# Optimization experiments

Hardware: AMD Instinct MI355X
Metric: run time of the kernel (lower is better)

## Reference

```python
import jax, jax.numpy as jnp
import numpy as np

EPS = 1e-5
BETA = 0.2

def _conv(x, w, b, stride, pad):
    y = jax.lax.conv_general_dilated(x, w, (stride, stride), ((pad, pad), (pad, pad)),
                                     dimension_numbers=('NCHW', 'OIHW', 'NCHW'))
    return y + b[None, :, None, None]

def _convT(x, w, b, stride, pad_eq):
    # PyTorch ConvTranspose2d(k=4, s=2, p=1) == dilated conv with lhs_dilation=s,
    # padding k-1-p=2, with the (already generated) equivalent OIHW kernel.
    y = jax.lax.conv_general_dilated(x, w, (1, 1), ((pad_eq, pad_eq), (pad_eq, pad_eq)),
                                     lhs_dilation=(stride, stride),
                                     dimension_numbers=('NCHW', 'OIHW', 'NCHW'))
    return y + b[None, :, None, None]

def _bn(x, g, b):
    # training-mode BatchNorm2d: batch statistics over (N,H,W), biased variance
    m = jnp.mean(x, axis=(0, 2, 3), keepdims=True)
    v = jnp.mean((x - m) ** 2, axis=(0, 2, 3), keepdims=True)
    return g[None, :, None, None] * (x - m) * jax.lax.rsqrt(v + EPS) + b[None, :, None, None]

def setup_inputs() -> dict:
    key = jax.random.key(0)
    ks = jax.random.split(key, 12)
    d = {}
    d['x'] = jax.random.normal(ks[0], (64, 1, 256, 256), jnp.float32)
    d['enc_w1'] = jax.random.normal(ks[1], (16, 1, 4, 4), jnp.float32) * 0.1
    d['enc_b1'] = jnp.zeros((16,), jnp.float32)
    d['bn1_g'] = jnp.ones((16,), jnp.float32)
    d['bn1_b'] = jnp.zeros((16,), jnp.float32)
    d['enc_w2'] = jax.random.normal(ks[2], (4, 16, 4, 4), jnp.float32) * 0.05
    d['enc_b2'] = jnp.zeros((4,), jnp.float32)
    d['bn2_g'] = jnp.ones((4,), jnp.float32)
    d['bn2_b'] = jnp.zeros((4,), jnp.float32)
    d['pre_w'] = jax.random.normal(ks[3], (2, 4, 1, 1), jnp.float32) * 0.3
    d['pre_b'] = jnp.zeros((2,), jnp.float32)
    d['codebook'] = jax.random.normal(ks[4], (3, 2), jnp.float32)
    d['post_w'] = jax.random.normal(ks[5], (4, 2, 1, 1), jnp.float32) * 0.3
    d['post_b'] = jnp.zeros((4,), jnp.float32)
    d['dec_w1'] = jax.random.normal(ks[6], (16, 4, 4, 4), jnp.float32) * 0.1
    d['dec_b1'] = jnp.zeros((16,), jnp.float32)
    d['bn3_g'] = jnp.ones((16,), jnp.float32)
    d['bn3_b'] = jnp.zeros((16,), jnp.float32)
    d['dec_w2'] = jax.random.normal(ks[7], (1, 16, 4, 4), jnp.float32) * 0.1
    d['dec_b2'] = jnp.zeros((1,), jnp.float32)
    return d

def reference(x, enc_w1, enc_b1, bn1_g, bn1_b, enc_w2, enc_b2, bn2_g, bn2_b,
              pre_w, pre_b, codebook, post_w, post_b,
              dec_w1, dec_b1, bn3_g, bn3_b, dec_w2, dec_b2):
    # encoder
    h = jax.nn.relu(_bn(_conv(x, enc_w1, enc_b1, 2, 1), bn1_g, bn1_b))
    h = jax.nn.relu(_bn(_conv(h, enc_w2, enc_b2, 2, 1), bn2_g, bn2_b))
    z = _conv(h, pre_w, pre_b, 1, 0)                      # [B,2,H/4,W/4]
    B, C, H, W = z.shape
    zf = z.reshape(B, C, H * W).transpose(0, 2, 1)        # [B, N, C]
    # squared distances to codebook [K,C]; argmin same as cdist argmin
    d2 = (jnp.sum(zf ** 2, -1, keepdims=True)
          - 2.0 * jnp.einsum('bnc,kc->bnk', zf, codebook)
          + jnp.sum(codebook ** 2, -1))                   # [B,N,K]
    idx = jnp.argmin(d2, axis=-1)                         # [B,N]
    q = codebook[idx]                                     # [B,N,C]
    commitment_loss = jnp.mean((jax.lax.stop_gradient(q) - zf) ** 2)
    codebook_loss = jnp.mean((q - jax.lax.stop_gradient(zf)) ** 2)
    quantize_losses = codebook_loss + BETA * commitment_loss
    q_st = zf + jax.lax.stop_gradient(q - zf)             # straight-through
    q4d = q_st.transpose(0, 2, 1).reshape(B, C, H, W)
    # decoder
    h = _conv(q4d, post_w, post_b, 1, 0)
    h = jax.nn.relu(_bn(_convT(h, dec_w1, dec_b1, 2, 2), bn3_g, bn3_b))
    out = _convT(h, dec_w2, dec_b2, 2, 2)                 # [B,1,256,256]
    return out, quantize_losses
```

## Files before the change

kernel.cpp:

```cpp
#include <hip/hip_runtime.h>


__global__ __launch_bounds__(256) void k_conv1(
    const float* __restrict__ x, const float* __restrict__ w1,
    const float* __restrict__ b1, float* __restrict__ y1,
    float* __restrict__ part)
{
  __shared__ float s_w[256];
  __shared__ float s_b[16];
  const int tid = threadIdx.x;
  { int c = tid >> 4, k = tid & 15; s_w[k * 16 + c] = w1[c * 16 + k]; }
  if (tid < 16) s_b[tid] = b1[tid];
  __syncthreads();

  const int lane = tid & 63;
  const int cb = lane & 3;
  const int psl = lane >> 2;
  const int gwave = (blockIdx.x << 2) | (tid >> 6);
  const int base = gwave << 8;
  const int n = base >> 14;
  const float* xb = x + n * 65536;
  const float4* s_w4 = (const float4*)s_w;
  const float4 bv = ((const float4*)s_b)[cb];

  float lsum[4] = {0.f, 0.f, 0.f, 0.f}, lsq[4] = {0.f, 0.f, 0.f, 0.f};

#pragma unroll 1
  for (int i = 0; i < 16; ++i) {
    const int pos = base + (i << 4) + psl;
    const int r = pos & 16383;
    const int oh = r >> 7, ow = r & 127;
    const int ihb = oh * 2 - 1, iwb = ow * 2 - 1;

    float a0 = bv.x, a1 = bv.y, a2 = bv.z, a3 = bv.w;
#pragma unroll
    for (int kh = 0; kh < 4; ++kh) {
      int ih = ihb + kh; bool okh = (unsigned)ih < 256u;
#pragma unroll
      for (int kw = 0; kw < 4; ++kw) {
        int iw = iwb + kw;
        bool ok = okh && ((unsigned)iw < 256u);
        float v = ok ? xb[ih * 256 + iw] : 0.f;
        float4 wv = s_w4[(kh * 4 + kw) * 4 + cb];
        a0 = fmaf(v, wv.x, a0); a1 = fmaf(v, wv.y, a1);
        a2 = fmaf(v, wv.z, a2); a3 = fmaf(v, wv.w, a3);
      }
    }
    *(float4*)(y1 + (size_t)pos * 16 + cb * 4) = make_float4(a0, a1, a2, a3);
    lsum[0] += a0; lsum[1] += a1; lsum[2] += a2; lsum[3] += a3;
    lsq[0] = fmaf(a0, a0, lsq[0]); lsq[1] = fmaf(a1, a1, lsq[1]);
    lsq[2] = fmaf(a2, a2, lsq[2]); lsq[3] = fmaf(a3, a3, lsq[3]);
  }

#pragma unroll
  for (int j = 0; j < 4; ++j) {
    float sv = lsum[j], qv = lsq[j];
#pragma unroll
    for (int d = 4; d < 64; d <<= 1) { sv += __shfl_down(sv, d); qv += __shfl_down(qv, d); }
    if (lane < 4) {
      part[(lane * 4 + j) * 4096 + gwave]      = sv;
      part[(16 + lane * 4 + j) * 4096 + gwave] = qv;
    }
  }
}

template <int NCH, int NW>
__global__ __launch_bounds__(256) void k_bnredN(
    const float* __restrict__ part, const float* __restrict__ g,
    const float* __restrict__ bt, float* __restrict__ sc,
    float* __restrict__ sh, double invN)
{
  __shared__ double sd[256], sqd[256];
  const int c = blockIdx.x, tid = threadIdx.x;
  const float4* ps = (const float4*)(part + (size_t)c * NW);
  const float4* pq = (const float4*)(part + (size_t)(NCH + c) * NW);
  double S = 0.0, Q = 0.0;
#pragma unroll
  for (int i = 0; i < NW / 1024; ++i) {
    float4 v = ps[i * 256 + tid];
    S += (double)v.x + (double)v.y + (double)v.z + (double)v.w;
    float4 q = pq[i * 256 + tid];
    Q += (double)q.x + (double)q.y + (double)q.z + (double)q.w;
  }
  sd[tid] = S; sqd[tid] = Q;
  __syncthreads();
  for (int off = 128; off > 0; off >>= 1) {
    if (tid < off) { sd[tid] += sd[tid + off]; sqd[tid] += sqd[tid + off]; }
    __syncthreads();
  }
  if (tid == 0) {
    double mean = sd[0] * invN;
    double var  = sqd[0] * invN - mean * mean;
    float scale = (float)((double)g[c] / sqrt(var + 1e-5));
    sc[c] = scale;
    sh[c] = bt[c] - (float)mean * scale;
  }
}

__global__ __launch_bounds__(256) void k_conv2(
    const float* __restrict__ y1, const float* __restrict__ w2,
    const float* __restrict__ b2, const float* __restrict__ bnp,
    float* __restrict__ y2, float* __restrict__ part)
{
  __shared__ float s_w[1024];
  __shared__ float s_sc[16], s_sh[16];
  __shared__ float s_b[4];
  const int tid = threadIdx.x;
  for (int i = tid; i < 1024; i += 256) {
    int co = i & 3, ci = (i >> 2) & 15, k = i >> 6;
    int kh = k >> 2, kw = k & 3;
    s_w[i] = w2[((co * 16 + ci) * 4 + kh) * 4 + kw];
  }
  if (tid < 16) { s_sc[tid] = bnp[tid]; s_sh[tid] = bnp[16 + tid]; }
  if (tid < 4)  s_b[tid] = b2[tid];
  __syncthreads();

  const int bid = ((blockIdx.x & 7) << 9) | (blockIdx.x >> 3);
  const int lane = tid & 63;
  const int cb = lane & 3;
  const int psl = lane >> 2;
  const int gwave = (bid << 2) | (tid >> 6);
  const int pos = (gwave << 4) + psl;
  const int n = pos >> 12, r = pos & 4095;
  const int oh = r >> 6, ow = r & 63;
  const int ihb = oh * 2 - 1, iwb = ow * 2 - 1;
  const float* yb = y1 + (size_t)n * 262144;
  const float4* s_w4 = (const float4*)s_w;
  const float4 scv = ((const float4*)s_sc)[cb];
  const float4 shv = ((const float4*)s_sh)[cb];

  float acc0 = 0.f, acc1 = 0.f, acc2 = 0.f, acc3 = 0.f;

#pragma unroll
  for (int kh = 0; kh < 4; ++kh) {
    int ih = ihb + kh; bool okh = (unsigned)ih < 128u;
#pragma unroll
    for (int kw = 0; kw < 4; ++kw) {
      int iw = iwb + kw;
      bool ok = okh && ((unsigned)iw < 128u);
      if (ok) {
        float4 v = *(const float4*)(yb + (ih * 128 + iw) * 16 + (cb << 2));
        float a0 = fmaxf(fmaf(v.x, scv.x, shv.x), 0.f);
        float a1 = fmaxf(fmaf(v.y, scv.y, shv.y), 0.f);
        float a2 = fmaxf(fmaf(v.z, scv.z, shv.z), 0.f);
        float a3 = fmaxf(fmaf(v.w, scv.w, shv.w), 0.f);
        int kb = (((kh << 2) | kw) << 4) + (cb << 2);
        float4 w0 = s_w4[kb + 0];
        float4 w1 = s_w4[kb + 1];
        float4 w2v = s_w4[kb + 2];
        float4 w3 = s_w4[kb + 3];
        acc0 = fmaf(a0, w0.x, fmaf(a1, w1.x, fmaf(a2, w2v.x, fmaf(a3, w3.x, acc0))));
        acc1 = fmaf(a0, w0.y, fmaf(a1, w1.y, fmaf(a2, w2v.y, fmaf(a3, w3.y, acc1))));
        acc2 = fmaf(a0, w0.z, fmaf(a1, w1.z, fmaf(a2, w2v.z, fmaf(a3, w3.z, acc2))));
        acc3 = fmaf(a0, w0.w, fmaf(a1, w1.w, fmaf(a2, w2v.w, fmaf(a3, w3.w, acc3))));
      }
    }
  }
  acc0 += __shfl_xor(acc0, 1); acc0 += __shfl_xor(acc0, 2);
  acc1 += __shfl_xor(acc1, 1); acc1 += __shfl_xor(acc1, 2);
  acc2 += __shfl_xor(acc2, 1); acc2 += __shfl_xor(acc2, 2);
  acc3 += __shfl_xor(acc3, 1); acc3 += __shfl_xor(acc3, 2);
  acc0 += s_b[0]; acc1 += s_b[1]; acc2 += s_b[2]; acc3 += s_b[3];

  if (cb == 0)
    *(float4*)(y2 + (size_t)pos * 4) = make_float4(acc0, acc1, acc2, acc3);

  float ls[4] = {acc0, acc1, acc2, acc3};
#pragma unroll
  for (int c = 0; c < 4; ++c) {
    float sv = ls[c], qv = ls[c] * ls[c];
#pragma unroll
    for (int d = 4; d < 64; d <<= 1) { sv += __shfl_down(sv, d); qv += __shfl_down(qv, d); }
    if (lane == 0) {
      part[c * 16384 + gwave]       = sv;
      part[(4 + c) * 16384 + gwave] = qv;
    }
  }
}

__global__ __launch_bounds__(256) void k_vq(
    const float* __restrict__ y2, const float* __restrict__ bnp2,
    const float* __restrict__ pw, const float* __restrict__ pb,
    const float* __restrict__ cb, const float* __restrict__ postw,
    const float* __restrict__ postb, float* __restrict__ h3,
    float* __restrict__ lpart)
{
  const int tid = threadIdx.x;
  const int pos = blockIdx.x * 256 + tid;
  float4 v = *(const float4*)(y2 + (size_t)pos * 4);
  float aa0 = fmaxf(fmaf(v.x, bnp2[0], bnp2[4]), 0.f);
  float aa1 = fmaxf(fmaf(v.y, bnp2[1], bnp2[5]), 0.f);
  float aa2 = fmaxf(fmaf(v.z, bnp2[2], bnp2[6]), 0.f);
  float aa3 = fmaxf(fmaf(v.w, bnp2[3], bnp2[7]), 0.f);
  float z0 = pb[0] + aa0*pw[0] + aa1*pw[1] + aa2*pw[2] + aa3*pw[3];
  float z1 = pb[1] + aa0*pw[4] + aa1*pw[5] + aa2*pw[6] + aa3*pw[7];

  float best = 3.4e38f, q0 = 0.f, q1 = 0.f;
#pragma unroll
  for (int k = 0; k < 3; ++k) {
    float c0 = cb[2 * k], c1 = cb[2 * k + 1];
    float dx = z0 - c0, dy = z1 - c1;
    float d = dx * dx + dy * dy;
    if (d < best) { best = d; q0 = c0; q1 = c1; }
  }
  float dl = (q0 - z0) * (q0 - z0) + (q1 - z1) * (q1 - z1);

  float4 hv;
  hv.x = fmaf(q0, postw[0], fmaf(q1, postw[1], postb[0]));
  hv.y = fmaf(q0, postw[2], fmaf(q1, postw[3], postb[1]));
  hv.z = fmaf(q0, postw[4], fmaf(q1, postw[5], postb[2]));
  hv.w = fmaf(q0, postw[6], fmaf(q1, postw[7], postb[3]));
  *(float4*)(h3 + (size_t)pos * 4) = hv;

  float s = dl;
#pragma unroll
  for (int d = 32; d > 0; d >>= 1) s += __shfl_down(s, d);
  __shared__ float ws4[4];
  if ((tid & 63) == 0) ws4[tid >> 6] = s;
  __syncthreads();
  if (tid == 0) lpart[blockIdx.x] = (ws4[0] + ws4[1]) + (ws4[2] + ws4[3]);
}

__global__ __launch_bounds__(256) void k_lossfin(
    const float* __restrict__ lpart, float* __restrict__ outp)
{
  const int tid = threadIdx.x;
  float s = lpart[tid] + lpart[tid + 256] + lpart[tid + 512] + lpart[tid + 768];
#pragma unroll
  for (int d = 32; d > 0; d >>= 1) s += __shfl_down(s, d);
  __shared__ float ws4[4];
  if ((tid & 63) == 0) ws4[tid >> 6] = s;
  __syncthreads();
  if (tid == 0) {
    double tot = (double)ws4[0] + (double)ws4[1] + (double)ws4[2] + (double)ws4[3];
    outp[0] = (float)(1.2 * tot / 524288.0);
  }
}

__global__ __launch_bounds__(256) void k_convt1(
    const float* __restrict__ h3, const float* __restrict__ w,
    const float* __restrict__ bias, float* __restrict__ h4,
    float* __restrict__ part)
{
  __shared__ float s_w[1024];
  __shared__ float s_b[16];
  const int tid = threadIdx.x;
  for (int i = tid; i < 1024; i += 256) {
    int co = i & 15, ci = (i >> 4) & 3, k = i >> 6;
    int kh = k >> 2, kw = k & 3;
    s_w[i] = w[((co * 4 + ci) * 4 + kh) * 4 + kw];
  }
  if (tid < 16) s_b[tid] = bias[tid];
  __syncthreads();

  const int lane = tid & 63;
  const int cb = lane & 3;
  const int psl = lane >> 2;
  const int gwave = (blockIdx.x << 2) | (tid >> 6);
  const int base = gwave << 8;
  const int n = base >> 14;
  const float* hb = h3 + (size_t)n * 16384;
  const float4* s_w4 = (const float4*)s_w;
  const float4 bv = ((const float4*)s_b)[cb];

  float lsum[4] = {0.f, 0.f, 0.f, 0.f}, lsq[4] = {0.f, 0.f, 0.f, 0.f};

#pragma unroll 1
  for (int i = 0; i < 16; ++i) {
    const int pos = base + (i << 4) + psl;
    const int r = pos & 16383;
    const int oh = r >> 7, ow = r & 127;
    const int ohp = oh & 1, owp = ow & 1;

    float a0 = bv.x, a1 = bv.y, a2 = bv.z, a3 = bv.w;
#pragma unroll
    for (int th = 0; th < 2; ++th) {
      int kh = th * 2 + ohp;
      int ih = (oh + kh - 2) >> 1;
      bool okh = (unsigned)ih < 64u;
#pragma unroll
      for (int tw = 0; tw < 2; ++tw) {
        int kw = tw * 2 + owp;
        int iw = (ow + kw - 2) >> 1;
        bool ok = okh && ((unsigned)iw < 64u);
        if (ok) {
          float4 v = *(const float4*)(hb + (ih * 64 + iw) * 4);
          int k16 = (kh * 4 + kw) * 16;
          float4 w0 = s_w4[k16 + 0 * 4 + cb];
          float4 w1 = s_w4[k16 + 1 * 4 + cb];
          float4 w2 = s_w4[k16 + 2 * 4 + cb];
          float4 w3 = s_w4[k16 + 3 * 4 + cb];
          a0 = fmaf(v.x, w0.x, fmaf(v.y, w1.x, fmaf(v.z, w2.x, fmaf(v.w, w3.x, a0))));
          a1 = fmaf(v.x, w0.y, fmaf(v.y, w1.y, fmaf(v.z, w2.y, fmaf(v.w, w3.y, a1))));
          a2 = fmaf(v.x, w0.z, fmaf(v.y, w1.z, fmaf(v.z, w2.z, fmaf(v.w, w3.z, a2))));
          a3 = fmaf(v.x, w0.w, fmaf(v.y, w1.w, fmaf(v.z, w2.w, fmaf(v.w, w3.w, a3))));
        }
      }
    }
    *(float4*)(h4 + (size_t)pos * 16 + cb * 4) = make_float4(a0, a1, a2, a3);
    lsum[0] += a0; lsum[1] += a1; lsum[2] += a2; lsum[3] += a3;
    lsq[0] = fmaf(a0, a0, lsq[0]); lsq[1] = fmaf(a1, a1, lsq[1]);
    lsq[2] = fmaf(a2, a2, lsq[2]); lsq[3] = fmaf(a3, a3, lsq[3]);
  }

#pragma unroll
  for (int j = 0; j < 4; ++j) {
    float sv = lsum[j], qv = lsq[j];
#pragma unroll
    for (int d = 4; d < 64; d <<= 1) { sv += __shfl_down(sv, d); qv += __shfl_down(qv, d); }
    if (lane < 4) {
      part[(lane * 4 + j) * 4096 + gwave]      = sv;
      part[(16 + lane * 4 + j) * 4096 + gwave] = qv;
    }
  }
}

__global__ __launch_bounds__(256) void k_convt2(
    const float* __restrict__ h4, const float* __restrict__ w,
    const float* __restrict__ bias, const float* __restrict__ bnp,
    float* __restrict__ out)
{
  __shared__ float4 s_t[4][18][19];
  __shared__ float s_w[256];
  const int tid = threadIdx.x;
  s_w[tid] = w[tid];

  const int bx = ((blockIdx.x & 7) << 9) | (blockIdx.x >> 3);
  const int n = bx >> 6;
  const int tile = bx & 63;
  const int ta = ((tile >> 3) << 4);
  const int tb = ((tile & 7) << 4);
  const float* hb = h4 + (size_t)n * 262144;

  for (int i = tid; i < 1296; i += 256) {
    int g = i & 3, p = i >> 2;
    int row = p / 18, col = p - row * 18;
    int ih = ta - 1 + row, iw = tb - 1 + col;
    float4 t = make_float4(0.f, 0.f, 0.f, 0.f);
    if (((unsigned)ih < 128u) && ((unsigned)iw < 128u)) {
      float4 v   = *(const float4*)(hb + ((ih << 7) + iw) * 16 + (g << 2));
      float4 scv = *(const float4*)(bnp + 40 + (g << 2));
      float4 shv = *(const float4*)(bnp + 56 + (g << 2));
      t.x = fmaxf(fmaf(v.x, scv.x, shv.x), 0.f);
      t.y = fmaxf(fmaf(v.y, scv.y, shv.y), 0.f);
      t.z = fmaxf(fmaf(v.z, scv.z, shv.z), 0.f);
      t.w = fmaxf(fmaf(v.w, scv.w, shv.w), 0.f);
    }
    s_t[g][row][col] = t;
  }
  __syncthreads();

  const int a = tid >> 4, b = tid & 15;
  const float4* s_w4 = (const float4*)s_w;
  float acc00 = 0.f, acc01 = 0.f, acc10 = 0.f, acc11 = 0.f;

#pragma unroll
  for (int g = 0; g < 4; ++g) {
    float4 v00 = s_t[g][a  ][b  ], v01 = s_t[g][a  ][b+1], v02 = s_t[g][a  ][b+2];
    float4 v10 = s_t[g][a+1][b  ], v11 = s_t[g][a+1][b+1], v12 = s_t[g][a+1][b+2];
    float4 v20 = s_t[g][a+2][b  ], v21 = s_t[g][a+2][b+1], v22 = s_t[g][a+2][b+2];
#pragma unroll
    for (int j = 0; j < 4; ++j) {
      int ci = g * 4 + j;
      float4 r0 = s_w4[ci*4+0], r1 = s_w4[ci*4+1];
      float4 r2 = s_w4[ci*4+2], r3 = s_w4[ci*4+3];
      float a00 = (j==0)?v00.x:(j==1)?v00.y:(j==2)?v00.z:v00.w;
      float a01 = (j==0)?v01.x:(j==1)?v01.y:(j==2)?v01.z:v01.w;
      float a02 = (j==0)?v02.x:(j==1)?v02.y:(j==2)?v02.z:v02.w;
      float a10 = (j==0)?v10.x:(j==1)?v10.y:(j==2)?v10.z:v10.w;
      float a11 = (j==0)?v11.x:(j==1)?v11.y:(j==2)?v11.z:v11.w;
      float a12 = (j==0)?v12.x:(j==1)?v12.y:(j==2)?v12.z:v12.w;
      float a20 = (j==0)?v20.x:(j==1)?v20.y:(j==2)?v20.z:v20.w;
      float a21 = (j==0)?v21.x:(j==1)?v21.y:(j==2)?v21.z:v21.w;
      float a22 = (j==0)?v22.x:(j==1)?v22.y:(j==2)?v22.z:v22.w;
      acc00 += a00*r0.x + a01*r0.z + a10*r2.x + a11*r2.z;
      acc01 += a01*r0.y + a02*r0.w + a11*r2.y + a12*r2.w;
      acc10 += a10*r1.x + a11*r1.z + a20*r3.x + a21*r3.z;
      acc11 += a11*r1.y + a12*r1.w + a21*r3.y + a22*r3.w;
    }
  }
  const float bv = bias[0];
  const int A = ta + a, B = tb + b;
  float* ob = out + n * 65536 + (2 * A) * 256 + 2 * B;
  *(float2*)ob         = make_float2(acc00 + bv, acc01 + bv);
  *(float2*)(ob + 256) = make_float2(acc10 + bv, acc11 + bv);
}

extern "C" void kernel_launch(void* const* d_in, const int* in_sizes, int n_in,
                              void* d_out, int out_size, void* d_ws, size_t ws_size,
                              hipStream_t stream)
{
  const float* x      = (const float*)d_in[0];
  const float* enc_w1 = (const float*)d_in[1];
  const float* enc_b1 = (const float*)d_in[2];
  const float* bn1_g  = (const float*)d_in[3];
  const float* bn1_b  = (const float*)d_in[4];
  const float* enc_w2 = (const float*)d_in[5];
  const float* enc_b2 = (const float*)d_in[6];
  const float* bn2_g  = (const float*)d_in[7];
  const float* bn2_b  = (const float*)d_in[8];
  const float* pre_w  = (const float*)d_in[9];
  const float* pre_b  = (const float*)d_in[10];
  const float* cb     = (const float*)d_in[11];
  const float* post_w = (const float*)d_in[12];
  const float* post_b = (const float*)d_in[13];
  const float* dec_w1 = (const float*)d_in[14];
  const float* dec_b1 = (const float*)d_in[15];
  const float* bn3_g  = (const float*)d_in[16];
  const float* bn3_b  = (const float*)d_in[17];
  const float* dec_w2 = (const float*)d_in[18];
  const float* dec_b2 = (const float*)d_in[19];

  float* ws  = (float*)d_ws;
  float* y1  = ws;
  float* y2  = ws + 16777216;
  float* h3  = ws + 17825792;
  float* p1  = ws + 18874368;
  float* p2  = ws + 19005440;
  float* lp  = ws + 19136512;
  float* bnp = ws + 19137536;
  float* h4  = y1;
  float* p3  = p1;
  float* out = (float*)d_out;

  k_conv1<<<1024, 256, 0, stream>>>(x, enc_w1, enc_b1, y1, p1);
  k_bnredN<16, 4096><<<16, 256, 0, stream>>>(p1, bn1_g, bn1_b, bnp, bnp + 16, 1.0 / 1048576.0);
  k_conv2<<<4096, 256, 0, stream>>>(y1, enc_w2, enc_b2, bnp, y2, p2);
  k_bnredN<4, 16384><<<4, 256, 0, stream>>>(p2, bn2_g, bn2_b, bnp + 32, bnp + 36, 1.0 / 262144.0);
  k_vq<<<1024, 256, 0, stream>>>(y2, bnp + 32, pre_w, pre_b, cb, post_w, post_b, h3, lp);
  k_lossfin<<<1, 256, 0, stream>>>(lp, out + 4194304);
  k_convt1<<<1024, 256, 0, stream>>>(h3, dec_w1, dec_b1, h4, p3);
  k_bnredN<16, 4096><<<16, 256, 0, stream>>>(p3, bn3_g, bn3_b, bnp + 40, bnp + 56, 1.0 / 1048576.0);
  k_convt2<<<4096, 256, 0, stream>>>(h4, dec_w2, dec_b2, bnp, out);
}
```

Measured before the change: 135.2 us.

## Recompute first transposed conv inside second to avoid h4 round-trip

The first decoder transposed conv now only computes batch-norm statistics and no longer writes its 64x128x128x16 output. The second transposed-conv kernel stages a small h3 tile in shared memory and recomputes the convT1 values for its halo tile before applying BN+ReLU. This removes a large global write and read of h4 (about 64MB each way) in exchange for computing convT1 twice, plus extra halo recompute and more shared memory per block.

After: 150.5 us. +11.3%, slower.

```diff
diff --git a/kernel.cpp b/kernel.cpp
--- a/kernel.cpp
+++ b/kernel.cpp
@@ -237,10 +237,9 @@
   }
 }
 
-__global__ __launch_bounds__(256) void k_convt1(
+__global__ __launch_bounds__(256) void k_convt1s(
     const float* __restrict__ h3, const float* __restrict__ w,
-    const float* __restrict__ bias, float* __restrict__ h4,
-    float* __restrict__ part)
+    const float* __restrict__ bias, float* __restrict__ part)
 {
   __shared__ float s_w[1024];
   __shared__ float s_b[16];
@@ -297,7 +296,6 @@
         }
       }
     }
-    *(float4*)(h4 + (size_t)pos * 16 + cb * 4) = make_float4(a0, a1, a2, a3);
     lsum[0] += a0; lsum[1] += a1; lsum[2] += a2; lsum[3] += a3;
     lsq[0] = fmaf(a0, a0, lsq[0]); lsq[1] = fmaf(a1, a1, lsq[1]);
     lsq[2] = fmaf(a2, a2, lsq[2]); lsq[3] = fmaf(a3, a3, lsq[3]);
@@ -315,22 +313,46 @@
   }
 }
 
-__global__ __launch_bounds__(256) void k_convt2(
-    const float* __restrict__ h4, const float* __restrict__ w,
-    const float* __restrict__ bias, const float* __restrict__ bnp,
+__global__ __launch_bounds__(256) void k_convt2f(
+    const float* __restrict__ h3, const float* __restrict__ w1,
+    const float* __restrict__ b1, const float* __restrict__ w2,
+    const float* __restrict__ bias2, const float* __restrict__ bnp,
     float* __restrict__ out)
 {
+  __shared__ float4 s_h3[11][12];
   __shared__ float4 s_t[4][18][19];
-  __shared__ float s_w[256];
-  const int tid = threadIdx.x;
-  s_w[tid] = w[tid];
+  __shared__ float s_w1[1024];
+  __shared__ float s_w2[256];
+  __shared__ float s_b1[16];
+  const int tid = threadIdx.x;
+  for (int i = tid; i < 1024; i += 256) {
+    int co = i & 15, ci = (i >> 4) & 3, k = i >> 6;
+    int kh = k >> 2, kw = k & 3;
+    s_w1[i] = w1[((co * 4 + ci) * 4 + kh) * 4 + kw];
+  }
+  s_w2[tid] = w2[tid];
+  if (tid < 16) s_b1[tid] = b1[tid];
 
   const int bx = ((blockIdx.x & 7) << 9) | (blockIdx.x >> 3);
   const int n = bx >> 6;
   const int tile = bx & 63;
   const int ta = ((tile >> 3) << 4);
   const int tb = ((tile & 7) << 4);
-  const float* hb = h4 + (size_t)n * 262144;
+  const int hrow0 = (ta >> 1) - 2, hcol0 = (tb >> 1) - 2;
+  const float* hb = h3 + (size_t)n * 16384;
+
+  if (tid < 121) {
+    int pr = tid / 11, pc = tid - pr * 11;
+    int sr = hrow0 + pr, sc = hcol0 + pc;
+    float4 t = make_float4(0.f, 0.f, 0.f, 0.f);
+    if (((unsigned)sr < 64u) && ((unsigned)sc < 64u))
+      t = *(const float4*)(hb + (sr * 64 + sc) * 4);
+    s_h3[pr][pc] = t;
+  }
+  __syncthreads();
+
+  const float4* s_w14 = (const float4*)s_w1;
+  const float4* s_b14 = (const float4*)s_b1;
 
   for (int i = tid; i < 1296; i += 256) {
     int g = i & 3, p = i >> 2;
@@ -338,20 +360,41 @@
     int ih = ta - 1 + row, iw = tb - 1 + col;
     float4 t = make_float4(0.f, 0.f, 0.f, 0.f);
     if (((unsigned)ih < 128u) && ((unsigned)iw < 128u)) {
-      float4 v   = *(const float4*)(hb + ((ih << 7) + iw) * 16 + (g << 2));
+      t = s_b14[g];
+      const int ohp = ih & 1, owp = iw & 1;
+#pragma unroll
+      for (int th = 0; th < 2; ++th) {
+        int kh = th * 2 + ohp;
+        int lr = ((ih + kh - 2) >> 1) - hrow0;
+#pragma unroll
+        for (int tw = 0; tw < 2; ++tw) {
+          int kw = tw * 2 + owp;
+          int lc = ((iw + kw - 2) >> 1) - hcol0;
+          float4 hv = s_h3[lr][lc];
+          int k16 = ((kh << 2) | kw) << 4;
+          float4 w0 = s_w14[k16 + 0 + g];
+          float4 w1v = s_w14[k16 + 4 + g];
+          float4 w2v = s_w14[k16 + 8 + g];
+          float4 w3v = s_w14[k16 + 12 + g];
+          t.x = fmaf(hv.x, w0.x, fmaf(hv.y, w1v.x, fmaf(hv.z, w2v.x, fmaf(hv.w, w3v.x, t.x))));
+          t.y = fmaf(hv.x, w0.y, fmaf(hv.y, w1v.y, fmaf(hv.z, w2v.y, fmaf(hv.w, w3v.y, t.y))));
+          t.z = fmaf(hv.x, w0.z, fmaf(hv.y, w1v.z, fmaf(hv.z, w2v.z, fmaf(hv.w, w3v.z, t.z))));
+          t.w = fmaf(hv.x, w0.w, fmaf(hv.y, w1v.w, fmaf(hv.z, w2v.w, fmaf(hv.w, w3v.w, t.w))));
+        }
+      }
       float4 scv = *(const float4*)(bnp + 40 + (g << 2));
       float4 shv = *(const float4*)(bnp + 56 + (g << 2));
-      t.x = fmaxf(fmaf(v.x, scv.x, shv.x), 0.f);
-      t.y = fmaxf(fmaf(v.y, scv.y, shv.y), 0.f);
-      t.z = fmaxf(fmaf(v.z, scv.z, shv.z), 0.f);
-      t.w = fmaxf(fmaf(v.w, scv.w, shv.w), 0.f);
+      t.x = fmaxf(fmaf(t.x, scv.x, shv.x), 0.f);
+      t.y = fmaxf(fmaf(t.y, scv.y, shv.y), 0.f);
+      t.z = fmaxf(fmaf(t.z, scv.z, shv.z), 0.f);
+      t.w = fmaxf(fmaf(t.w, scv.w, shv.w), 0.f);
     }
     s_t[g][row][col] = t;
   }
   __syncthreads();
 
   const int a = tid >> 4, b = tid & 15;
-  const float4* s_w4 = (const float4*)s_w;
+  const float4* s_w4 = (const float4*)s_w2;
   float acc00 = 0.f, acc01 = 0.f, acc10 = 0.f, acc11 = 0.f;
 
 #pragma unroll
@@ -379,7 +422,7 @@
       acc11 += a11*r1.y + a12*r1.w + a21*r3.y + a22*r3.w;
     }
   }
-  const float bv = bias[0];
+  const float bv = bias2[0];
   const int A = ta + a, B = tb + b;
   float* ob = out + n * 65536 + (2 * A) * 256 + 2 * B;
   *(float2*)ob         = make_float2(acc00 + bv, acc01 + bv);
@@ -419,7 +462,6 @@
   float* p2  = ws + 19005440;
   float* lp  = ws + 19136512;
   float* bnp = ws + 19137536;
-  float* h4  = y1;
   float* p3  = p1;
   float* out = (float*)d_out;
 
@@ -429,7 +471,7 @@
   k_bnredN<4, 16384><<<4, 256, 0, stream>>>(p2, bn2_g, bn2_b, bnp + 32, bnp + 36, 1.0 / 262144.0);
   k_vq<<<1024, 256, 0, stream>>>(y2, bnp + 32, pre_w, pre_b, cb, post_w, post_b, h3, lp);
   k_lossfin<<<1, 256, 0, stream>>>(lp, out + 4194304);
-  k_convt1<<<1024, 256, 0, stream>>>(h3, dec_w1, dec_b1, h4, p3);
+  k_convt1s<<<1024, 256, 0, stream>>>(h3, dec_w1, dec_b1, p3);
   k_bnredN<16, 4096><<<16, 256, 0, stream>>>(p3, bn3_g, bn3_b, bnp + 40, bnp + 56, 1.0 / 1048576.0);
-  k_convt2<<<4096, 256, 0, stream>>>(h4, dec_w2, dec_b2, bnp, out);
-}
+  k_convt2f<<<4096, 256, 0, stream>>>(h3, dec_w1, dec_b1, dec_w2, dec_b2, bnp, out);
+}
```
